# Kernel optimization log

Measured on AMD Instinct MI355X. Metric: run time of the kernel, lower is better.

Reference implementation:

```python
import jax, jax.numpy as jnp
import numpy as np

IOU_THRESH = 0.1
TEACHER_CONF = 0.2
EPS = 1e-7


def box_iou(box1, box2, giou=False):
    # box1: [B,m,4], box2: [B,n,4] in cxcywh -> pairwise IoU [B,m,n]
    b1 = box1[:, :, None, :]  # [B,m,1,4]
    b2 = box2[:, None, :, :]  # [B,1,n,4]
    x1, y1, w1, h1 = b1[..., 0], b1[..., 1], b1[..., 2], b1[..., 3]
    x2, y2, w2, h2 = b2[..., 0], b2[..., 1], b2[..., 2], b2[..., 3]
    b1x1, b1x2, b1y1, b1y2 = x1 - w1 / 2, x1 + w1 / 2, y1 - h1 / 2, y1 + h1 / 2
    b2x1, b2x2, b2y1, b2y2 = x2 - w2 / 2, x2 + w2 / 2, y2 - h2 / 2, y2 + h2 / 2
    inter = (jnp.maximum(jnp.minimum(b1x2, b2x2) - jnp.maximum(b1x1, b2x1), 0.0)
             * jnp.maximum(jnp.minimum(b1y2, b2y2) - jnp.maximum(b1y1, b2y1), 0.0))
    union = w1 * h1 + w2 * h2 - inter + EPS
    iou = inter / union
    if giou:
        c_area = ((jnp.maximum(b1x2, b2x2) - jnp.minimum(b1x1, b2x1))
                  * (jnp.maximum(b1y2, b2y2) - jnp.minimum(b1y1, b2y1)) + EPS)
        return iou - (c_area - union) / c_area
    return iou


def setup_inputs() -> dict:
    key = jax.random.key(0)
    k1, k2, k3, k4 = jax.random.split(key, 4)
    B, Q, C = 16, 900, 80
    return {
        "s_pred_logits": jax.random.normal(k1, (B, Q, C), dtype=jnp.float32),
        "s_pred_boxes": jax.random.uniform(k2, (B, Q, 4), dtype=jnp.float32),
        "t_pred_logits": jax.random.normal(k3, (B, Q, C), dtype=jnp.float32),
        "t_pred_boxes": jax.random.uniform(k4, (B, Q, 4), dtype=jnp.float32),
        "target_nums": 128,
    }


def reference(s_pred_logits, s_pred_boxes, t_pred_logits, t_pred_boxes, target_nums):
    B, Q, C = s_pred_logits.shape
    tn = jnp.asarray(target_nums, dtype=s_pred_logits.dtype)

    # teacher confidence flag (detached in original; bool => no grad anyway)
    conf = jax.nn.sigmoid(t_pred_logits).max(-1) > TEACHER_CONF  # [B,Q]

    # pairwise IoU and best-teacher match per student query
    iou = box_iou(s_pred_boxes, t_pred_boxes)        # [B,Q,Q]
    max_iou = iou.max(-1)                            # [B,Q]
    max_idx = jnp.argmax(iou, -1)                    # [B,Q]

    # torch: gather((max_iou>th).repeat & conf_flag, 1, idx[...,None]) reads column 0
    flag = jnp.take_along_axis(max_iou > IOU_THRESH, max_idx, axis=1) & conf[:, 0:1]  # [B,Q]

    # torch gathers column 0 of the pairwise L1 / GIoU matrices -> only t_boxes[:,0] matters
    l1_col0 = jnp.abs(s_pred_boxes - t_pred_boxes[:, 0:1, :]).sum(-1)               # [B,Q]
    giou_col0 = 1.0 - box_iou(s_pred_boxes, t_pred_boxes[:, 0:1, :], giou=True)[:, :, 0]  # [B,Q]
    l1_g = jnp.take_along_axis(l1_col0, max_idx, axis=1)
    giou_g = jnp.take_along_axis(giou_col0, max_idx, axis=1)

    lbox_l1 = jnp.where(flag, l1_g, 0.0).sum() / tn * 5.0
    lbox_iou = jnp.where(flag, giou_g, 0.0).sum() / tn * 2.0

    # pairwise BCE over flattened [B*Q] rows; torch gather picks column max_idx_flat[p]
    # (indexes rows 0..Q-1 of the flattened teacher -- faithfully reproduced)
    s_flat = s_pred_logits.reshape(B * Q, C)
    t_flat = t_pred_logits.reshape(B * Q, C)
    idx_flat = max_idx.reshape(-1)                   # values in [0,Q)
    t_probs = jax.nn.sigmoid(t_flat[idx_flat])       # [B*Q, C]
    # BCEWithLogits(x, t) = softplus(x) - x*t  (stable)
    bce = jax.nn.softplus(s_flat) - s_flat * t_probs
    lcls = bce.mean(-1).sum() / tn

    loss = lbox_l1 + lbox_iou + lcls
    return jnp.where(conf.any(), loss, 0.0)
```

## Files before the change

kernel.cpp:

```cpp
#include <hip/hip_runtime.h>
#include <math.h>

#define NB 16
#define NQ 900
#define NC 80
#define EPSV 1e-7f
#define IOU_THR 0.1f
#define SPB 16
#define CHB 57

__device__ __forceinline__ float sigm(float x) { return 1.0f / (1.0f + __expf(-x)); }

__global__ __launch_bounds__(256) void k_main(
    const float* __restrict__ s_logits,
    const float* __restrict__ s_boxes,
    const float* __restrict__ t_logits,
    const float* __restrict__ t_boxes,
    int*    __restrict__ g_idx,
    float*  __restrict__ g_v,
    float2* __restrict__ g_part)
{
    __shared__ float4 tcor[NQ];
    __shared__ float  tarea[NQ];
    __shared__ int    lidx[SPB];
    __shared__ float  sconf0;
    __shared__ float2 spart[4];

    const int bx  = blockIdx.x;
    const int b   = blockIdx.y;
    const int tid = threadIdx.x;

    const float4* tb = (const float4*)(t_boxes + b * NQ * 4);
    for (int i = tid; i < NQ; i += 256) {
        float4 t = tb[i];
        float hw = t.z * 0.5f, hh = t.w * 0.5f;
        tcor[i]  = make_float4(t.x - hw, t.x + hw, t.y - hh, t.y + hh);
        tarea[i] = t.z * t.w;
    }
    if (tid < 64) {
        const float* tl = t_logits + b * NQ * NC;
        float m = tl[tid];
        if (tid < NC - 64) m = fmaxf(m, tl[tid + 64]);
        for (int s = 32; s >= 1; s >>= 1) m = fmaxf(m, __shfl_xor(m, s, 64));
        if (tid == 0) sconf0 = (sigm(m) > 0.2f) ? 1.0f : 0.0f;
    }
    __syncthreads();

    const int s  = tid >> 4;
    const int tc = tid & 15;
    const int sq = bx * SPB + s;
    const bool act = (sq < NQ);
    float best = -1.0f; int bidx = 0;
    float4 sb = make_float4(0.f, 0.f, 0.f, 0.f);
    float sx1 = 0.f, sx2 = 0.f, sy1 = 0.f, sy2 = 0.f, sarea = 0.f;
    if (act) {
        sb = ((const float4*)(s_boxes + b * NQ * 4))[sq];
        float shw = sb.z * 0.5f, shh = sb.w * 0.5f;
        sx1 = sb.x - shw; sx2 = sb.x + shw;
        sy1 = sb.y - shh; sy2 = sb.y + shh;
        sarea = sb.z * sb.w;
        #pragma unroll 4
        for (int i = 0; i < 57; ++i) {
            int t = tc + (i << 4);
            if (t < NQ) {
                float4 c = tcor[t];
                float iw = fminf(sx2, c.y) - fmaxf(sx1, c.x);
                float ih = fminf(sy2, c.w) - fmaxf(sy1, c.z);
                float inter = fmaxf(iw, 0.0f) * fmaxf(ih, 0.0f);
                float uni = sarea + tarea[t] - inter + EPSV;
                float iou = inter * __frcp_rn(uni);
                if (iou > best) { best = iou; bidx = t; }
            }
        }
    }
    for (int m = 1; m <= 8; m <<= 1) {
        float ov = __shfl_xor(best, m, 64);
        int   oi = __shfl_xor(bidx, m, 64);
        if (ov > best || (ov == best && oi < bidx)) { best = ov; bidx = oi; }
    }
    if (act && tc == 0) {
        int o = b * NQ + sq;
        g_idx[o] = bidx;
        lidx[s]  = bidx;
        float4 t0 = tb[0];
        float4 c  = tcor[0];
        float iw = fminf(sx2, c.y) - fmaxf(sx1, c.x);
        float ih = fminf(sy2, c.w) - fmaxf(sy1, c.z);
        float inter = fmaxf(iw, 0.0f) * fmaxf(ih, 0.0f);
        float uni = sarea + tarea[0] - inter + EPSV;
        float iou = inter / uni;
        float cw = fmaxf(sx2, c.y) - fminf(sx1, c.x);
        float ch = fmaxf(sy2, c.w) - fminf(sy1, c.z);
        float carea = cw * ch + EPSV;
        float giou1 = 1.0f - (iou - (carea - uni) / carea);
        float l1 = fabsf(sb.x - t0.x) + fabsf(sb.y - t0.y) +
                   fabsf(sb.z - t0.z) + fabsf(sb.w - t0.w);
        float v = 0.0f;
        if (sconf0 > 0.0f && best > IOU_THR) v = 5.0f * l1 + 2.0f * giou1;
        g_v[o] = v;
    }
    __syncthreads();

    const int wv = tid >> 6, lane = tid & 63;
    float bcea = 0.f, confb = 0.f;
    #pragma unroll
    for (int k = 0; k < 4; ++k) {
        int s2  = wv * 4 + k;
        int sq2 = bx * SPB + s2;
        if (sq2 < NQ) {
            int row = b * NQ + sq2;
            int j   = lidx[s2];
            const float* srow = s_logits + row * NC;
            const float* trow = t_logits + row * NC;
            const float* grow = t_logits + j * NC;
            float s0 = srow[lane], t0 = trow[lane], g0 = grow[lane];
            float bce = fmaxf(s0, 0.f) + __logf(1.0f + __expf(-fabsf(s0)))
                      - s0 * __frcp_rn(1.0f + __expf(-g0));
            float tmax = t0;
            if (lane < NC - 64) {
                float s1 = srow[lane + 64], t1 = trow[lane + 64], g1 = grow[lane + 64];
                bce += fmaxf(s1, 0.f) + __logf(1.0f + __expf(-fabsf(s1)))
                     - s1 * __frcp_rn(1.0f + __expf(-g1));
                tmax = fmaxf(tmax, t1);
            }
            for (int sft = 32; sft >= 1; sft >>= 1) {
                bce  += __shfl_xor(bce, sft, 64);
                tmax  = fmaxf(tmax, __shfl_xor(tmax, sft, 64));
            }
            if (lane == 0) {
                bcea += bce * (1.0f / (float)NC);
                if (sigm(tmax) > 0.2f) confb = 1.0f;
            }
        }
    }
    if (lane == 0) spart[wv] = make_float2(bcea, confb);
    __syncthreads();
    if (tid == 0) {
        float2 a = spart[0], bq = spart[1], c = spart[2], d = spart[3];
        g_part[b * CHB + bx] = make_float2(a.x + bq.x + c.x + d.x,
                                           fmaxf(fmaxf(a.y, bq.y), fmaxf(c.y, d.y)));
    }
}

__global__ __launch_bounds__(1024) void k_final(
    const int*    __restrict__ g_idx,
    const float*  __restrict__ g_v,
    const float2* __restrict__ g_part,
    const int*    __restrict__ tn_p,
    float* __restrict__ out)
{
    const int tid = threadIdx.x;
    float bs = 0.f, ca = 0.f;
    if (tid < NB * CHB) { float2 p = g_part[tid]; bs = p.x; ca = p.y; }
    float vs = 0.f;
    #pragma unroll
    for (int k = 0; k < 15; ++k) {
        int i = tid + k * 1024;
        if (i < NB * NQ) {
            int j = g_idx[i];
            int b = i / NQ;
            vs += g_v[b * NQ + j];
        }
    }
    __shared__ float rb[16], rv[16], rc[16];
    const int wv = tid >> 6, lane = tid & 63;
    for (int m = 32; m >= 1; m >>= 1) {
        bs += __shfl_xor(bs, m, 64);
        vs += __shfl_xor(vs, m, 64);
        ca  = fmaxf(ca, __shfl_xor(ca, m, 64));
    }
    if (lane == 0) { rb[wv] = bs; rv[wv] = vs; rc[wv] = ca; }
    __syncthreads();
    if (tid == 0) {
        float sb = 0.f, sv = 0.f, sc = 0.f;
        for (int k = 0; k < 16; ++k) { sb += rb[k]; sv += rv[k]; sc = fmaxf(sc, rc[k]); }
        float tn = (float)tn_p[0];
        out[0] = (sc > 0.f) ? (sv + sb) / tn : 0.0f;
    }
}

extern "C" void kernel_launch(void* const* d_in, const int* in_sizes, int n_in,
                              void* d_out, int out_size, void* d_ws, size_t ws_size,
                              hipStream_t stream) {
    const float* s_logits = (const float*)d_in[0];
    const float* s_boxes  = (const float*)d_in[1];
    const float* t_logits = (const float*)d_in[2];
    const float* t_boxes  = (const float*)d_in[3];
    const int*   tn       = (const int*)d_in[4];
    float* out = (float*)d_out;

    char* ws = (char*)d_ws;
    int*    g_idx  = (int*)(ws);
    float*  g_v    = (float*)(ws + 57600);
    float2* g_part = (float2*)(ws + 115200);

    k_main<<<dim3(CHB, NB), 256, 0, stream>>>(s_logits, s_boxes, t_logits, t_boxes,
                                              g_idx, g_v, g_part);
    k_final<<<1, 1024, 0, stream>>>(g_idx, g_v, g_part, tn, out);
}
```

Before: 31.88 us.

## Replace gather of v with per-target histogram; spread BCE rows across 16-lane groups

Instead of storing per-query argmax indices and gathering g_v in the final kernel, each query atomically increments a count for its matched teacher index, and the final kernel computes the sum of count times v with coalesced reads. The BCE phase now gives each query row to a 16-lane group handling 5 columns, so all four rows per wave run at once instead of looping with 16 idle lanes. This adds a memset launch and global atomics in exchange for removing the indirect gather.

```diff
diff --git a/kernel.cpp b/kernel.cpp
--- a/kernel.cpp
+++ b/kernel.cpp
@@ -16,7 +16,7 @@
     const float* __restrict__ s_boxes,
     const float* __restrict__ t_logits,
     const float* __restrict__ t_boxes,
-    int*    __restrict__ g_idx,
+    int*    __restrict__ g_cnt,
     float*  __restrict__ g_v,
     float2* __restrict__ g_part)
 {
@@ -24,11 +24,13 @@
     __shared__ float  tarea[NQ];
     __shared__ int    lidx[SPB];
     __shared__ float  sconf0;
-    __shared__ float2 spart[4];
+    __shared__ float2 sres[SPB];
 
     const int bx  = blockIdx.x;
     const int b   = blockIdx.y;
     const int tid = threadIdx.x;
+
+    if (tid < SPB) sres[tid] = make_float2(0.f, 0.f);
 
     const float4* tb = (const float4*)(t_boxes + b * NQ * 4);
     for (int i = tid; i < NQ; i += 256) {
@@ -80,8 +82,8 @@
     }
     if (act && tc == 0) {
         int o = b * NQ + sq;
-        g_idx[o] = bidx;
-        lidx[s]  = bidx;
+        lidx[s] = bidx;
+        atomicAdd(&g_cnt[b * NQ + bidx], 1);
         float4 t0 = tb[0];
         float4 c  = tcor[0];
         float iw = fminf(sx2, c.y) - fmaxf(sx1, c.x);
@@ -101,49 +103,44 @@
     }
     __syncthreads();
 
-    const int wv = tid >> 6, lane = tid & 63;
-    float bcea = 0.f, confb = 0.f;
-    #pragma unroll
-    for (int k = 0; k < 4; ++k) {
-        int s2  = wv * 4 + k;
-        int sq2 = bx * SPB + s2;
-        if (sq2 < NQ) {
-            int row = b * NQ + sq2;
-            int j   = lidx[s2];
-            const float* srow = s_logits + row * NC;
-            const float* trow = t_logits + row * NC;
-            const float* grow = t_logits + j * NC;
-            float s0 = srow[lane], t0 = trow[lane], g0 = grow[lane];
-            float bce = fmaxf(s0, 0.f) + __logf(1.0f + __expf(-fabsf(s0)))
-                      - s0 * __frcp_rn(1.0f + __expf(-g0));
-            float tmax = t0;
-            if (lane < NC - 64) {
-                float s1 = srow[lane + 64], t1 = trow[lane + 64], g1 = grow[lane + 64];
-                bce += fmaxf(s1, 0.f) + __logf(1.0f + __expf(-fabsf(s1)))
-                     - s1 * __frcp_rn(1.0f + __expf(-g1));
-                tmax = fmaxf(tmax, t1);
-            }
-            for (int sft = 32; sft >= 1; sft >>= 1) {
-                bce  += __shfl_xor(bce, sft, 64);
-                tmax  = fmaxf(tmax, __shfl_xor(tmax, sft, 64));
-            }
-            if (lane == 0) {
-                bcea += bce * (1.0f / (float)NC);
-                if (sigm(tmax) > 0.2f) confb = 1.0f;
-            }
+    const int wv  = tid >> 6, lane = tid & 63;
+    const int grp = lane >> 4, tc2 = lane & 15;
+    const int s2  = wv * 4 + grp;
+    const int sq2 = bx * SPB + s2;
+    if (sq2 < NQ) {
+        int row = b * NQ + sq2;
+        int j   = lidx[s2];
+        const float* srow = s_logits + row * NC;
+        const float* trow = t_logits + row * NC;
+        const float* grow = t_logits + j * NC;
+        float bce = 0.f, tmax = -1e30f;
+        #pragma unroll
+        for (int e = 0; e < 5; ++e) {
+            int c = e * 16 + tc2;
+            float s0 = srow[c], t0 = trow[c], g0 = grow[c];
+            bce += fmaxf(s0, 0.f) + __logf(1.0f + __expf(-fabsf(s0)))
+                 - s0 * __frcp_rn(1.0f + __expf(-g0));
+            tmax = fmaxf(tmax, t0);
         }
+        for (int m = 8; m >= 1; m >>= 1) {
+            bce  += __shfl_xor(bce, m, 64);
+            tmax  = fmaxf(tmax, __shfl_xor(tmax, m, 64));
+        }
+        if (tc2 == 0)
+            sres[s2] = make_float2(bce * (1.0f / (float)NC),
+                                   (sigm(tmax) > 0.2f) ? 1.0f : 0.0f);
     }
-    if (lane == 0) spart[wv] = make_float2(bcea, confb);
     __syncthreads();
     if (tid == 0) {
-        float2 a = spart[0], bq = spart[1], c = spart[2], d = spart[3];
-        g_part[b * CHB + bx] = make_float2(a.x + bq.x + c.x + d.x,
-                                           fmaxf(fmaxf(a.y, bq.y), fmaxf(c.y, d.y)));
+        float bs = 0.f, ca = 0.f;
+        #pragma unroll
+        for (int k = 0; k < SPB; ++k) { bs += sres[k].x; ca = fmaxf(ca, sres[k].y); }
+        g_part[b * CHB + bx] = make_float2(bs, ca);
     }
 }
 
 __global__ __launch_bounds__(1024) void k_final(
-    const int*    __restrict__ g_idx,
+    const int*    __restrict__ g_cnt,
     const float*  __restrict__ g_v,
     const float2* __restrict__ g_part,
     const int*    __restrict__ tn_p,
@@ -156,11 +153,7 @@
     #pragma unroll
     for (int k = 0; k < 15; ++k) {
         int i = tid + k * 1024;
-        if (i < NB * NQ) {
-            int j = g_idx[i];
-            int b = i / NQ;
-            vs += g_v[b * NQ + j];
-        }
+        if (i < NB * NQ) vs += (float)g_cnt[i] * g_v[i];
     }
     __shared__ float rb[16], rv[16], rc[16];
     const int wv = tid >> 6, lane = tid & 63;
@@ -190,11 +183,12 @@
     float* out = (float*)d_out;
 
     char* ws = (char*)d_ws;
-    int*    g_idx  = (int*)(ws);
+    int*    g_cnt  = (int*)(ws);
     float*  g_v    = (float*)(ws + 57600);
     float2* g_part = (float2*)(ws + 115200);
 
+    hipMemsetAsync(g_cnt, 0, NB * NQ * sizeof(int), stream);
     k_main<<<dim3(CHB, NB), 256, 0, stream>>>(s_logits, s_boxes, t_logits, t_boxes,
-                                              g_idx, g_v, g_part);
-    k_final<<<1, 1024, 0, stream>>>(g_idx, g_v, g_part, tn, out);
+                                              g_cnt, g_v, g_part);
+    k_final<<<1, 1024, 0, stream>>>(g_cnt, g_v, g_part, tn, out);
 }
```

New measurement: 30.53 us. 1.04x faster.
